# Kernel optimization log

Hardware: AMD Instinct MI355X
Metric: run time of the kernel (lower is better)

Reference implementation:

```python
import jax, jax.numpy as jnp
import numpy as np

T, B, L, CTX, H = 512, 512, 16, 64, 128
STATE_DIM, SHOT, PID, DATA = 32, 12, 35, 23


def setup_inputs() -> dict:
    key = jax.random.key(0)
    ks = jax.random.split(key, 64)
    k = iter(ks)
    def rn(shape, s=0.1):
        return (jax.random.normal(next(k), shape) * s).astype(jnp.float32)
    xs = jax.random.normal(next(k), (T, B, DATA), jnp.float32)
    xs = xs.at[:, :, 12].set(jax.random.randint(next(k), (T, B), 0, SHOT).astype(jnp.float32))
    xs = xs.at[:, :, 17].set(jax.random.randint(next(k), (T, B), 0, PID).astype(jnp.float32))
    xs = xs.at[:, :, 20].set(jax.random.randint(next(k), (T, B), 0, SHOT).astype(jnp.float32))
    return dict(
        total_xs=jnp.zeros((1,), jnp.float32),
        xs=xs,
        ts=jnp.linspace(0.0, 2.0, T).astype(jnp.float32),
        noise_std=jnp.asarray(0.1, jnp.float32),
        z0_noise=jax.random.normal(next(k), (B, L), jnp.float32),
        bm_noise=jax.random.normal(next(k), (T - 1, B, L), jnp.float32),
        shot_emb=rn((SHOT, 8)), player_emb=rn((PID, 8)),
        gru_wih=rn((3 * H, STATE_DIM)), gru_whh=rn((3 * H, H)),
        gru_bih=rn((3 * H,)), gru_bhh=rn((3 * H,)),
        enc_w=rn((CTX, H)), enc_b=rn((CTX,)),
        qz0_w=rn((2 * L, CTX)), qz0_b=rn((2 * L,)),
        f_w1=rn((H, L + CTX)), f_b1=rn((H,)), f_w2=rn((H, H)), f_b2=rn((H,)),
        f_w3=rn((L, H)), f_b3=rn((L,)),
        h_w1=rn((H, L)), h_b1=rn((H,)), h_w2=rn((H, H)), h_b2=rn((H,)),
        h_w3=rn((L, H)), h_b3=rn((L,)),
        g_w1=rn((L, H)), g_b1=rn((L, H)), g_w2=rn((L, H)), g_b2=rn((L,)),
        proj_w=rn((STATE_DIM, L)), proj_b=rn((STATE_DIM,)),
        pz0_mean=jnp.zeros((1, L), jnp.float32), pz0_logstd=jnp.zeros((1, L), jnp.float32),
        act_w=rn((128, L)), act_b=rn((128,)),
        act_land_w=rn((2, 128)), act_shot_w=rn((SHOT, 128)), act_move_w=rn((2, 128)),
    )


def _forward(xs, noise_std, shot_emb, player_emb, gru_wih, gru_whh, gru_bih, gru_bhh,
             enc_w, enc_b, qz0_w, qz0_b,
             f_w1, f_b1, f_w2, f_b2, f_w3, f_b3,
             h_w1, h_b1, h_w2, h_b2, h_w3, h_b3,
             g_w1, g_b1, g_w2, g_b2,
             proj_w, proj_b, pz0_mean, pz0_logstd,
             act_w, act_b, act_land_w, act_shot_w, act_move_w,
             ts, z0_noise, bm_noise):
    # --- SDE_embed_and_transform: replace shot/player id cols with embeddings ---
    state = xs[:, :, :18]
    shot_ids = state[:, :, 12].astype(jnp.int32)
    pid_ids = state[:, :, 17].astype(jnp.int32)
    state_t = jnp.concatenate([state[:, :, :12], shot_emb[shot_ids],
                               state[:, :, 13:17], player_emb[pid_ids]], axis=-1)  # (T,B,32)
    xs_t = jnp.concatenate([state_t, xs[:, :, 18:]], axis=-1)  # (T,B,37)
    # --- Encoder: GRU over time-reversed states, linear head, flip back ---
    def gru_step(h, xt):
        gi = xt @ gru_wih.T + gru_bih
        gh = h @ gru_whh.T + gru_bhh
        ir, iz, inn = jnp.split(gi, 3, axis=-1)
        hr, hz, hn = jnp.split(gh, 3, axis=-1)
        r = jax.nn.sigmoid(ir + hr)
        zg = jax.nn.sigmoid(iz + hz)
        n = jnp.tanh(inn + r * hn)
        hnew = (1.0 - zg) * n + zg * h
        return hnew, hnew
    h0 = jnp.zeros((xs.shape[1], gru_whh.shape[1]), xs.dtype)
    _, hs = jax.lax.scan(gru_step, h0, state_t[::-1])
    ctx = (hs @ enc_w.T + enc_b)[::-1]  # (T,B,CTX)
    # --- posterior z0 ---
    qm, qls = jnp.split(ctx[0] @ qz0_w.T + qz0_b, 2, axis=1)
    z0 = qm + jnp.exp(qls) * z0_noise
    # --- Euler-Maruyama with logqp; searchsorted(right) -> ctx[min(i+1,T-1)] = ctx[i+1] ---
    dts = ts[1:] - ts[:-1]  # (T-1,)
    dW = jnp.sqrt(dts)[:, None, None] * bm_noise
    ctx_steps = ctx[1:]
    def mlp3(x, w1, b1, w2, b2, w3, b3):
        h1 = jax.nn.softplus(x @ w1.T + b1)
        h2 = jax.nn.softplus(h1 @ w2.T + b2)
        return h2 @ w3.T + b3
    def g_diag(y):  # (B,L): per-latent-dim scalar nets, batched over L
        hg = jax.nn.softplus(y[:, :, None] * g_w1[None] + g_b1[None])  # (B,L,H)
        return jax.nn.sigmoid(jnp.einsum('blh,lh->bl', hg, g_w2) + g_b2)
    def sde_step(z, inp):
        c, dw, dt = inp
        f_val = mlp3(jnp.concatenate([z, c], axis=1), f_w1, f_b1, f_w2, f_b2, f_w3, f_b3)
        h_val = mlp3(z, h_w1, h_b1, h_w2, h_b2, h_w3, h_b3)
        g_val = g_diag(z)
        u = (f_val - h_val) / g_val
        logr = 0.5 * jnp.sum(u * u, axis=1) * dt
        z_new = z + f_val * dt + g_val * dw
        return z_new, (z_new, logr)
    _, (z_tail, log_ratio) = jax.lax.scan(sde_step, z0, (ctx_steps, dW, dts))
    zs = jnp.concatenate([z0[None], z_tail], axis=0)  # (T,B,L)
    _xs = zs @ proj_w.T + proj_b  # (T,B,32)
    # --- action model losses ---
    a = jax.nn.relu(zs @ act_w.T + act_b)
    land = (a @ act_land_w.T).reshape(-1, 2)
    shot_logits = (a @ act_shot_w.T).reshape(-1, act_shot_w.shape[0])
    move = (a @ act_move_w.T).reshape(-1, 2)
    true_actions = xs_t[:, :, -5:]
    true_land = true_actions[:, :, :2].reshape(-1, 2)
    true_move = true_actions[:, :, 3:].reshape(-1, 2)
    true_shot = true_actions[:, :, 2].astype(jnp.int32).reshape(-1)
    land_loss = jnp.mean((land - true_land) ** 2)
    move_loss = jnp.mean((move - true_move) ** 2)
    logp = jax.nn.log_softmax(shot_logits, axis=-1)
    picked = jnp.take_along_axis(logp, true_shot[:, None], axis=1)[:, 0]
    mask = (true_shot != 0).astype(logp.dtype)  # CrossEntropy ignore_index=0
    shot_loss = -jnp.sum(picked * mask) / jnp.maximum(jnp.sum(mask), 1.0)
    # --- reconstruction log-likelihood ---
    xs_state = xs_t[:, :, :STATE_DIM]
    LOG2PI = 1.8378770664093453
    log_pxs = jnp.mean(jnp.sum(
        -0.5 * ((xs_state - _xs) / noise_std) ** 2 - jnp.log(noise_std) - 0.5 * LOG2PI,
        axis=(0, 2)))
    # --- KL(q(z0) || p(z0)) ---
    var_q = jnp.exp(2.0 * qls)
    var_p = jnp.exp(2.0 * pz0_logstd)
    kl = pz0_logstd - qls + (var_q + (qm - pz0_mean) ** 2) / (2.0 * var_p) - 0.5
    logqp0 = jnp.mean(jnp.sum(kl, axis=1))
    logqp_path = jnp.mean(jnp.sum(log_ratio, axis=0))
    return log_pxs, logqp0 + logqp_path + land_loss + shot_loss + move_loss


def reference(total_xs, xs, ts, noise_std, z0_noise, bm_noise, shot_emb, player_emb,
              gru_wih, gru_whh, gru_bih, gru_bhh, enc_w, enc_b, qz0_w, qz0_b,
              f_w1, f_b1, f_w2, f_b2, f_w3, f_b3, h_w1, h_b1, h_w2, h_b2, h_w3, h_b3,
              g_w1, g_b1, g_w2, g_b2, proj_w, proj_b, pz0_mean, pz0_logstd,
              act_w, act_b, act_land_w, act_shot_w, act_move_w):
    return _forward(xs, noise_std, shot_emb, player_emb, gru_wih, gru_whh, gru_bih, gru_bhh,
                    enc_w, enc_b, qz0_w, qz0_b,
                    f_w1, f_b1, f_w2, f_b2, f_w3, f_b3,
                    h_w1, h_b1, h_w2, h_b2, h_w3, h_b3,
                    g_w1, g_b1, g_w2, g_b2,
                    proj_w, proj_b, pz0_mean, pz0_logstd,
                    act_w, act_b, act_land_w, act_shot_w, act_move_w,
                    ts, z0_noise, bm_noise)
```

## Files before the change

### kernel.cpp

```cpp
#include <hip/hip_runtime.h>
#include <cstdint>

typedef _Float16 f16;
typedef _Float16 f16x2 __attribute__((ext_vector_type(2)));

#define T_STEPS 512
#define B_SZ 512
#define LOG2PI 1.8378770664093453f

__device__ __forceinline__ void barrier_lds() {
  asm volatile("s_waitcnt lgkmcnt(0)" ::: "memory");
  __builtin_amdgcn_s_barrier();
  asm volatile("" ::: "memory");
}

__device__ __forceinline__ uint32_t packh2(float a, float b) {
  f16x2 v; v[0] = (f16)a; v[1] = (f16)b;
  return __builtin_bit_cast(uint32_t, v);
}

__device__ __forceinline__ float fdot2(uint32_t a, uint32_t b, float c) {
#if defined(__AMDGCN__) && __has_builtin(__builtin_amdgcn_fdot2)
  return __builtin_amdgcn_fdot2(__builtin_bit_cast(f16x2, a),
                                __builtin_bit_cast(f16x2, b), c, false);
#else
  f16x2 x = __builtin_bit_cast(f16x2, a), y = __builtin_bit_cast(f16x2, b);
  return c + (float)x[0] * (float)y[0] + (float)x[1] * (float)y[1];
#endif
}

#define DOT4(acc, w0, w1, w2, w3, v)                                     \
  do {                                                                   \
    acc = fdot2((w0), (v).x, acc); acc = fdot2((w1), (v).y, acc);        \
    acc = fdot2((w2), (v).z, acc); acc = fdot2((w3), (v).w, acc);        \
  } while (0)

__device__ __forceinline__ float sigmoidf_(float x) {
  return 1.0f / (1.0f + __expf(-x));
}
__device__ __forceinline__ float tanhf_(float x) {
  float ax = fabsf(x);
  float t = __expf(-2.0f * ax);
  float r = (1.0f - t) / (1.0f + t);
  return copysignf(r, x);
}
__device__ __forceinline__ float softplusf_(float x) {
  return fmaxf(x, 0.0f) + __logf(1.0f + __expf(-fabsf(x)));
}

__global__ __launch_bounds__(256) void k_embed(
    const float* __restrict__ xs, const float* __restrict__ shot_emb,
    const float* __restrict__ player_emb, f16* __restrict__ state_t,
    float* __restrict__ accums) {
  if (blockIdx.x == 0 && threadIdx.x < 16) accums[threadIdx.x] = 0.0f;
  size_t idx = (size_t)blockIdx.x * 256 + threadIdx.x;
  const float* xp = xs + idx * 23;
  f16* op = state_t + idx * 32;
  int sid = (int)xp[12];
  int pid = (int)xp[17];
#pragma unroll
  for (int i = 0; i < 12; ++i) op[i] = (f16)xp[i];
  const float* se = shot_emb + sid * 8;
#pragma unroll
  for (int i = 0; i < 8; ++i) op[12 + i] = (f16)se[i];
#pragma unroll
  for (int i = 0; i < 4; ++i) op[20 + i] = (f16)xp[13 + i];
  const float* pe = player_emb + pid * 8;
#pragma unroll
  for (int i = 0; i < 8; ++i) op[24 + i] = (f16)pe[i];
}

__global__ __launch_bounds__(256) void k_gtab(
    const float* __restrict__ gw1, const float* __restrict__ gb1,
    const float* __restrict__ gw2, const float* __restrict__ gb2,
    float* __restrict__ g_tab) {
  int gid = blockIdx.x * 256 + threadIdx.x;
  int l = gid >> 16, yi = gid & 0xffff;
  f16 hy = __builtin_bit_cast(f16, (unsigned short)yi);
  float y = (float)hy;
  const float* w1 = gw1 + l * 128;
  const float* b1 = gb1 + l * 128;
  const float* w2 = gw2 + l * 128;
  float a0 = 0.f, a1 = 0.f;
#pragma unroll 8
  for (int h = 0; h < 128; h += 2) {
    a0 = fmaf(softplusf_(fmaf(y, w1[h], b1[h])), w2[h], a0);
    a1 = fmaf(softplusf_(fmaf(y, w1[h + 1], b1[h + 1])), w2[h + 1], a1);
  }
  g_tab[gid] = sigmoidf_(a0 + a1 + gb2[l]);
}

__global__ __launch_bounds__(512) void k_gru(
    const f16* __restrict__ state_t, const float* __restrict__ wih,
    const float* __restrict__ whh, const float* __restrict__ bih,
    const float* __restrict__ bhh, const float* __restrict__ enc_w,
    const float* __restrict__ enc_b, const float* __restrict__ qz0_w,
    const float* __restrict__ qz0_b, const float* __restrict__ z0_noise,
    const float* __restrict__ pz0_mean, const float* __restrict__ pz0_logstd,
    f16* __restrict__ ctx, float* __restrict__ z0_out,
    float* __restrict__ accums) {
  __shared__ uint32_t s_x[2][16];
  __shared__ uint32_t s_h[2][64];
  __shared__ float s_gates[2 * 128 * 4];
  __shared__ float s_encp[2 * 64 * 2];
  __shared__ float s_ctx0[2][64];
  __shared__ float s_q[2][32];

  const int tid = threadIdx.x;
  const int bbase = blockIdx.x * 2;
  const uint32_t* stu = (const uint32_t*)state_t;

  uint32_t wA[64];
  uint32_t wB[16];
  float bias0 = 0.f, bias1 = 0.f, encbr = 0.f;

  if (tid < 256) {
    int g = tid >> 7, du = tid & 127;
    const float* whr = whh + (size_t)(g * 128 + du) * 128;
#pragma unroll
    for (int i = 0; i < 64; ++i) wA[i] = packh2(whr[2 * i], whr[2 * i + 1]);
    const float* wxr = wih + (size_t)(g * 128 + du) * 32;
#pragma unroll
    for (int i = 0; i < 16; ++i) wB[i] = packh2(wxr[2 * i], wxr[2 * i + 1]);
    bias0 = bih[g * 128 + du] + bhh[g * 128 + du];
  } else if (tid < 384) {
    int du = tid - 256;
    const float* whr = whh + (size_t)(256 + du) * 128;
#pragma unroll
    for (int i = 0; i < 64; ++i) wA[i] = packh2(whr[2 * i], whr[2 * i + 1]);
    const float* wxr = wih + (size_t)(256 + du) * 32;
#pragma unroll
    for (int i = 0; i < 16; ++i) wB[i] = packh2(wxr[2 * i], wxr[2 * i + 1]);
    bias0 = bih[256 + du];
    bias1 = bhh[256 + du];
  } else {
    int e = tid - 384, c = e & 63, ks = e >> 6;
    const float* wer = enc_w + (size_t)c * 128 + ks * 64;
#pragma unroll
    for (int i = 0; i < 32; ++i) wA[i] = packh2(wer[2 * i], wer[2 * i + 1]);
    encbr = enc_b[c];
  }

  if (tid < 128) s_h[tid >> 6][tid & 63] = 0u;
  if (tid < 32) {
    int b = tid >> 4, i = tid & 15;
    s_x[b][i] = stu[((size_t)(T_STEPS - 1) * B_SZ + bbase + b) * 16 + i];
  }
  float h_old = 0.0f;
  __syncthreads();

  for (int t = T_STEPS - 1; t >= 0; --t) {
    uint4 xpref = make_uint4(0, 0, 0, 0);
    if (tid < 256) {
      int g = tid >> 7, du = tid & 127;
#pragma unroll
      for (int b = 0; b < 2; ++b) {
        float a = bias0;
        const uint4* xq = (const uint4*)&s_x[b][0];
#pragma unroll
        for (int j = 0; j < 4; ++j) {
          uint4 v = xq[j];
          DOT4(a, wB[4 * j], wB[4 * j + 1], wB[4 * j + 2], wB[4 * j + 3], v);
        }
        const uint4* hq = (const uint4*)&s_h[b][0];
#pragma unroll
        for (int j = 0; j < 16; ++j) {
          uint4 v = hq[j];
          DOT4(a, wA[4 * j], wA[4 * j + 1], wA[4 * j + 2], wA[4 * j + 3], v);
        }
        s_gates[(b * 128 + du) * 4 + g] = a;
      }
    } else if (tid < 384) {
      int du = tid - 256;
#pragma unroll
      for (int b = 0; b < 2; ++b) {
        float aI = bias0, aH = bias1;
        const uint4* xq = (const uint4*)&s_x[b][0];
#pragma unroll
        for (int j = 0; j < 4; ++j) {
          uint4 v = xq[j];
          DOT4(aI, wB[4 * j], wB[4 * j + 1], wB[4 * j + 2], wB[4 * j + 3], v);
        }
        const uint4* hq = (const uint4*)&s_h[b][0];
#pragma unroll
        for (int j = 0; j < 16; ++j) {
          uint4 v = hq[j];
          DOT4(aH, wA[4 * j], wA[4 * j + 1], wA[4 * j + 2], wA[4 * j + 3], v);
        }
        s_gates[(b * 128 + du) * 4 + 2] = aI;
        s_gates[(b * 128 + du) * 4 + 3] = aH;
      }
    } else {
      int e = tid - 384, ks = e >> 6, cc = e & 63;
      (void)cc;
      if (t < T_STEPS - 1) {
#pragma unroll
        for (int b = 0; b < 2; ++b) {
          float a = 0.f;
          const uint4* hq = (const uint4*)&s_h[b][ks * 32];
#pragma unroll
          for (int j = 0; j < 8; ++j) {
            uint4 v = hq[j];
            DOT4(a, wA[4 * j], wA[4 * j + 1], wA[4 * j + 2], wA[4 * j + 3], v);
          }
          s_encp[(b * 64 + cc) * 2 + ks] = a;
        }
      }
      if (e < 8 && t > 0) {
        int b = e & 1, q = e >> 1;
        xpref = *(const uint4*)(stu +
                                ((size_t)(t - 1) * B_SZ + bbase + b) * 16 + q * 4);
      }
    }
    barrier_lds();
    if (tid < 256) {
      int b = tid >> 7, du = tid & 127;
      const float4 gt = *(const float4*)&s_gates[(b * 128 + du) * 4];
      float r = sigmoidf_(gt.x), zg = sigmoidf_(gt.y);
      float n = tanhf_(gt.z + r * gt.w);
      float hnew = (1.0f - zg) * n + zg * h_old;
      h_old = hnew;
      ((f16*)&s_h[b][0])[du] = (f16)hnew;
    } else if (tid >= 384) {
      int e = tid - 384, cc = e & 63, b = e >> 6;
      if (t < T_STEPS - 1) {
        float2 p = *(const float2*)&s_encp[(b * 64 + cc) * 2];
        ctx[((size_t)(t + 1) * B_SZ + bbase + b) * 64 + cc] =
            (f16)(p.x + p.y + encbr);
      }
      if (e < 8 && t > 0) {
        int b2 = e & 1, q = e >> 1;
        *(uint4*)&s_x[b2][q * 4] = xpref;
      }
    }
    barrier_lds();
  }

  if (tid >= 384) {
    int e = tid - 384, ks = e >> 6, cc = e & 63;
#pragma unroll
    for (int b = 0; b < 2; ++b) {
      float a = 0.f;
      const uint4* hq = (const uint4*)&s_h[b][ks * 32];
#pragma unroll
      for (int j = 0; j < 8; ++j) {
        uint4 v = hq[j];
        DOT4(a, wA[4 * j], wA[4 * j + 1], wA[4 * j + 2], wA[4 * j + 3], v);
      }
      s_encp[(b * 64 + cc) * 2 + ks] = a;
    }
  }
  __syncthreads();
  if (tid >= 384) {
    int e = tid - 384, cc = e & 63, b = e >> 6;
    float2 p = *(const float2*)&s_encp[(b * 64 + cc) * 2];
    float val = p.x + p.y + encbr;
    ctx[((size_t)bbase + b) * 64 + cc] = (f16)val;
    s_ctx0[b][cc] = val;
  }
  __syncthreads();
  if (tid < 64) {
    int b = tid >> 5, o = tid & 31;
    float acc = qz0_b[o];
#pragma unroll 8
    for (int k = 0; k < 64; ++k) acc += qz0_w[o * 64 + k] * s_ctx0[b][k];
    s_q[b][o] = acc;
  }
  __syncthreads();
  if (tid < 32) {
    int b = tid >> 4, l = tid & 15;
    int bg = bbase + b;
    float qm = s_q[b][l], qls = s_q[b][16 + l];
    float z0v = qm + __expf(qls) * z0_noise[bg * 16 + l];
    z0_out[bg * 16 + l] = z0v;
    float pm = pz0_mean[l], pls = pz0_logstd[l];
    float var_q = __expf(2.0f * qls);
    float var_p = __expf(2.0f * pls);
    float dm = qm - pm;
    float kl = pls - qls + (var_q + dm * dm) / (2.0f * var_p) - 0.5f;
    atomicAdd(&accums[5], kl);
  }
}

__global__ __launch_bounds__(256, 2) void k_sde(
    const f16* __restrict__ ctx, const float* __restrict__ z0_in,
    const float* __restrict__ ts, const float* __restrict__ bm_noise,
    const float* __restrict__ fw1, const float* __restrict__ fb1,
    const float* __restrict__ fw2, const float* __restrict__ fb2,
    const float* __restrict__ fw3, const float* __restrict__ fb3,
    const float* __restrict__ hw1, const float* __restrict__ hb1,
    const float* __restrict__ hw2, const float* __restrict__ hb2,
    const float* __restrict__ hw3, const float* __restrict__ hb3,
    const float* __restrict__ g_tab,
    f16* __restrict__ zs, float* __restrict__ accums) {
  __shared__ uint32_t s_x2[40];
  __shared__ uint32_t s_h1[2][64];
  __shared__ uint32_t s_h2[2][64];
  __shared__ float s_dts[T_STEPS];

  const int tid = threadIdx.x;
  const int bg = blockIdx.x;
  const uint32_t* cu = (const uint32_t*)ctx;
  const int l = tid >> 2;
  const bool zlane = (tid < 64) && ((tid & 3) == 0);

  uint32_t uw1[40];
  uint32_t wP2[64];
  uint32_t wP3[32];
  float bias1r = 0.f, bias2r = 0.f, fb3r = 0.f, hb3r = 0.f;

  if (tid < 128) {
    const float* w = fw1 + (size_t)tid * 80;
#pragma unroll
    for (int i = 0; i < 40; ++i) uw1[i] = packh2(w[2 * i], w[2 * i + 1]);
    bias1r = fb1[tid];
  } else {
    int u = tid - 128;
    const float* w = hw1 + (size_t)u * 16;
#pragma unroll
    for (int i = 0; i < 8; ++i) uw1[i] = packh2(w[2 * i], w[2 * i + 1]);
    bias1r = hb1[u];
  }
  {
    int mlp = tid >> 7, u = tid & 127;
    const float* w = (mlp ? hw2 : fw2) + (size_t)u * 128;
#pragma unroll
    for (int i = 0; i < 64; ++i) wP2[i] = packh2(w[2 * i], w[2 * i + 1]);
    bias2r = (mlp ? hb2 : fb2)[u];
  }
  if (tid < 64) {
    int mlp = (tid >> 1) & 1, kh = tid & 1;
    const float* w = (mlp ? hw3 : fw3) + (size_t)l * 128 + kh * 64;
#pragma unroll
    for (int i = 0; i < 32; ++i) wP3[i] = packh2(w[2 * i], w[2 * i + 1]);
    if ((tid & 3) == 0) {
      fb3r = fb3[l];
      hb3r = hb3[l];
    }
  }

  for (int i = tid; i < T_STEPS - 1; i += 256) s_dts[i] = ts[i + 1] - ts[i];
  float zreg = 0.f, bmc = 0.f, path_acc = 0.f;
  uint4 cpref = make_uint4(0, 0, 0, 0);
  if (zlane) {
    zreg = z0_in[bg * 16 + l];
    ((f16*)&s_x2[0])[l] = (f16)zreg;
    zs[(size_t)bg * 16 + l] = (f16)zreg;
    bmc = bm_noise[(size_t)bg * 16 + l];
  }
  if (tid >= 128 && tid < 136) {
    int q = tid - 128;
    uint4 v = *(const uint4*)(cu + ((size_t)1 * B_SZ + bg) * 32 + q * 4);
    *(uint4*)&s_x2[8 + q * 4] = v;
  }
  __syncthreads();

  for (int t = 0; t < T_STEPS - 1; ++t) {
    float bmn = 0.f, gvp = 0.f;
    if (zlane) {
      unsigned short zb = __builtin_bit_cast(unsigned short, (f16)zreg);
      gvp = g_tab[l * 65536 + (int)zb];
      if (t < T_STEPS - 2)
        bmn = bm_noise[((size_t)(t + 1) * B_SZ + bg) * 16 + l];
    }
    if (tid >= 128 && tid < 136 && t <= T_STEPS - 3) {
      int q = tid - 128;
      cpref = *(const uint4*)(cu + ((size_t)(t + 2) * B_SZ + bg) * 32 + q * 4);
    }
    if (tid < 128) {
      float a0 = bias1r, a1 = 0.f;
      const uint4* xq = (const uint4*)&s_x2[0];
#pragma unroll
      for (int j = 0; j < 10; j += 2) {
        uint4 v0 = xq[j], v1 = xq[j + 1];
        DOT4(a0, uw1[4 * j], uw1[4 * j + 1], uw1[4 * j + 2], uw1[4 * j + 3], v0);
        DOT4(a1, uw1[4 * j + 4], uw1[4 * j + 5], uw1[4 * j + 6], uw1[4 * j + 7], v1);
      }
      ((f16*)&s_h1[0][0])[tid] = (f16)softplusf_(a0 + a1);
    } else {
      float a = bias1r;
      const uint4* xq = (const uint4*)&s_x2[0];
#pragma unroll
      for (int j = 0; j < 2; ++j) {
        uint4 v = xq[j];
        DOT4(a, uw1[4 * j], uw1[4 * j + 1], uw1[4 * j + 2], uw1[4 * j + 3], v);
      }
      ((f16*)&s_h1[1][0])[tid - 128] = (f16)softplusf_(a);
    }
    barrier_lds();
    {
      int mlp = tid >> 7, u = tid & 127;
      float a0 = 0.f, a1 = 0.f;
      const uint4* hq = (const uint4*)&s_h1[mlp][0];
#pragma unroll
      for (int j = 0; j < 16; j += 2) {
        uint4 v0 = hq[j], v1 = hq[j + 1];
        DOT4(a0, wP2[4 * j], wP2[4 * j + 1], wP2[4 * j + 2], wP2[4 * j + 3], v0);
        DOT4(a1, wP2[4 * j + 4], wP2[4 * j + 5], wP2[4 * j + 6], wP2[4 * j + 7], v1);
      }
      ((f16*)&s_h2[mlp][0])[u] = (f16)softplusf_(a0 + a1 + bias2r);
    }
    barrier_lds();
    if (tid < 64) {
      int kh = tid & 1;
      int mlp = (tid >> 1) & 1;
      const uint4* hq = (const uint4*)&s_h2[mlp][kh * 32];
      float a0 = 0.f, a1 = 0.f;
#pragma unroll
      for (int j = 0; j < 8; j += 2) {
        uint4 v0 = hq[j], v1 = hq[j + 1];
        DOT4(a0, wP3[4 * j], wP3[4 * j + 1], wP3[4 * j + 2], wP3[4 * j + 3], v0);
        DOT4(a1, wP3[4 * j + 4], wP3[4 * j + 5], wP3[4 * j + 6], wP3[4 * j + 7], v1);
      }
      float a = a0 + a1;
      float full = a + __shfl_xor(a, 1);
      float other = __shfl_xor(full, 2);
      if ((tid & 3) == 0) {
        float fv = full + fb3r;
        float hv = other + hb3r;
        float gv = gvp;
        float dt = s_dts[t];
        float u_ = (fv - hv) / gv;
        float lsum = u_ * u_;
        lsum += __shfl_xor(lsum, 4);
        lsum += __shfl_xor(lsum, 8);
        lsum += __shfl_xor(lsum, 16);
        lsum += __shfl_xor(lsum, 32);
        if (tid == 0) path_acc += 0.5f * lsum * dt;
        float dw = sqrtf(dt) * bmc;
        float zn = zreg + fv * dt + gv * dw;
        zreg = zn;
        ((f16*)&s_x2[0])[l] = (f16)zn;
        zs[((size_t)(t + 1) * B_SZ + bg) * 16 + l] = (f16)zn;
        bmc = bmn;
      }
    } else if (tid >= 128 && tid < 136 && t <= T_STEPS - 3) {
      int q = tid - 128;
      *(uint4*)&s_x2[8 + q * 4] = cpref;
    }
    barrier_lds();
  }
  if (tid == 0) atomicAdd(&accums[6], path_acc);
}

__global__ __launch_bounds__(256) void k_dec(
    const f16* __restrict__ zs, const f16* __restrict__ state_t,
    const float* __restrict__ xs, const float* __restrict__ proj_w,
    const float* __restrict__ proj_b, const float* __restrict__ act_w,
    const float* __restrict__ act_b, const float* __restrict__ land_w,
    const float* __restrict__ shot_w, const float* __restrict__ move_w,
    float* __restrict__ accums) {
  __shared__ uint32_t s_proj[8 * 32];
  __shared__ uint32_t s_act[8 * 128];
  __shared__ uint32_t s_head[128 * 8];
  __shared__ float s_pb[32], s_ab[128];
  __shared__ float s_red[4 * 5];

  const int tid = threadIdx.x;
  for (int id = tid; id < 8 * 32; id += 256) {
    int kp = id & 7, n = id >> 3;
    s_proj[kp * 32 + n] = packh2(proj_w[n * 16 + 2 * kp], proj_w[n * 16 + 2 * kp + 1]);
  }
  for (int id = tid; id < 8 * 128; id += 256) {
    int kp = id & 7, n = id >> 3;
    s_act[kp * 128 + n] = packh2(act_w[n * 16 + 2 * kp], act_w[n * 16 + 2 * kp + 1]);
  }
  for (int id = tid; id < 128 * 8; id += 256) {
    int j = id >> 3, p = id & 7;
    int h0 = 2 * p, h1 = 2 * p + 1;
    float w0 = (h0 < 2) ? land_w[h0 * 128 + j]
                        : (h0 < 14 ? shot_w[(h0 - 2) * 128 + j]
                                   : move_w[(h0 - 14) * 128 + j]);
    float w1 = (h1 < 2) ? land_w[h1 * 128 + j]
                        : (h1 < 14 ? shot_w[(h1 - 2) * 128 + j]
                                   : move_w[(h1 - 14) * 128 + j]);
    s_head[j * 8 + p] = packh2(w0, w1);
  }
  if (tid < 32) s_pb[tid] = proj_b[tid];
  if (tid < 128) s_ab[tid] = act_b[tid];
  __syncthreads();

  size_t idx = (size_t)blockIdx.x * 256 + tid;
  uint32_t z2[8];
  const uint32_t* zp = (const uint32_t*)(zs + idx * 16);
#pragma unroll
  for (int i = 0; i < 8; ++i) z2[i] = zp[i];
  uint32_t stv[16];
  const uint32_t* stp = (const uint32_t*)(state_t + idx * 32);
#pragma unroll
  for (int i = 0; i < 16; ++i) stv[i] = stp[i];

  float sqsum = 0.0f;
#pragma unroll 4
  for (int i = 0; i < 32; ++i) {
    float acc = s_pb[i];
#pragma unroll
    for (int kp = 0; kp < 8; ++kp) acc = fdot2(s_proj[kp * 32 + i], z2[kp], acc);
    f16x2 sv = __builtin_bit_cast(f16x2, stv[i >> 1]);
    float d = (float)sv[i & 1] - acc;
    sqsum += d * d;
  }

  float hd[16];
#pragma unroll
  for (int i = 0; i < 16; ++i) hd[i] = 0.0f;
#pragma unroll 2
  for (int j = 0; j < 128; ++j) {
    float a = s_ab[j];
#pragma unroll
    for (int kp = 0; kp < 8; ++kp) a = fdot2(s_act[kp * 128 + j], z2[kp], a);
    a = fmaxf(a, 0.0f);
#pragma unroll
    for (int p = 0; p < 8; ++p) {
      f16x2 w = __builtin_bit_cast(f16x2, s_head[j * 8 + p]);
      hd[2 * p] += (float)w[0] * a;
      hd[2 * p + 1] += (float)w[1] * a;
    }
  }
  const float* xp = xs + idx * 23;
  float dl0 = hd[0] - xp[18], dl1 = hd[1] - xp[19];
  float land = dl0 * dl0 + dl1 * dl1;
  float dm0 = hd[14] - xp[21], dm1 = hd[15] - xp[22];
  float move = dm0 * dm0 + dm1 * dm1;
  int sid = (int)xp[20];
  float m = hd[2];
#pragma unroll
  for (int s = 1; s < 12; ++s) m = fmaxf(m, hd[2 + s]);
  float sume = 0.0f;
#pragma unroll
  for (int s = 0; s < 12; ++s) sume += __expf(hd[2 + s] - m);
  float lse = m + __logf(sume);
  float pl = 0.0f;
#pragma unroll
  for (int s = 0; s < 12; ++s)
    if (s == sid) pl = hd[2 + s];
  float picked = 0.0f, cnt = 0.0f;
  if (sid != 0) {
    picked = pl - lse;
    cnt = 1.0f;
  }
  float vals[5] = {sqsum, land, move, picked, cnt};
#pragma unroll
  for (int v = 0; v < 5; ++v) {
    float x = vals[v];
    for (int off = 1; off < 64; off <<= 1) x += __shfl_xor(x, off);
    vals[v] = x;
  }
  int lane = tid & 63, wv = tid >> 6;
  if (lane == 0) {
#pragma unroll
    for (int v = 0; v < 5; ++v) s_red[wv * 5 + v] = vals[v];
  }
  __syncthreads();
  if (tid == 0) {
#pragma unroll
    for (int v = 0; v < 5; ++v) {
      float s = s_red[v] + s_red[5 + v] + s_red[10 + v] + s_red[15 + v];
      atomicAdd(&accums[v], s);
    }
  }
}

__global__ void k_fin(const float* __restrict__ accums,
                      const float* __restrict__ noise_std,
                      float* __restrict__ out) {
  if (threadIdx.x == 0 && blockIdx.x == 0) {
    float sd = noise_std[0];
    float log_pxs = -0.5f * accums[0] / (sd * sd * (float)B_SZ) -
                    (float)T_STEPS * 32.0f * (logf(sd) + 0.5f * LOG2PI);
    float land = accums[1] / (float)(T_STEPS * B_SZ * 2);
    float move = accums[2] / (float)(T_STEPS * B_SZ * 2);
    float shot = -accums[3] / fmaxf(accums[4], 1.0f);
    float out1 = accums[5] / (float)B_SZ + accums[6] / (float)B_SZ + land + shot + move;
    out[0] = log_pxs;
    out[1] = out1;
  }
}

extern "C" void kernel_launch(void* const* d_in, const int* in_sizes, int n_in,
                              void* d_out, int out_size, void* d_ws,
                              size_t ws_size, hipStream_t stream) {
  const float* xs = (const float*)d_in[1];
  const float* ts = (const float*)d_in[2];
  const float* noise_std = (const float*)d_in[3];
  const float* z0_noise = (const float*)d_in[4];
  const float* bm_noise = (const float*)d_in[5];
  const float* shot_emb = (const float*)d_in[6];
  const float* player_emb = (const float*)d_in[7];
  const float* gru_wih = (const float*)d_in[8];
  const float* gru_whh = (const float*)d_in[9];
  const float* gru_bih = (const float*)d_in[10];
  const float* gru_bhh = (const float*)d_in[11];
  const float* enc_w = (const float*)d_in[12];
  const float* enc_b = (const float*)d_in[13];
  const float* qz0_w = (const float*)d_in[14];
  const float* qz0_b = (const float*)d_in[15];
  const float* f_w1 = (const float*)d_in[16];
  const float* f_b1 = (const float*)d_in[17];
  const float* f_w2 = (const float*)d_in[18];
  const float* f_b2 = (const float*)d_in[19];
  const float* f_w3 = (const float*)d_in[20];
  const float* f_b3 = (const float*)d_in[21];
  const float* h_w1 = (const float*)d_in[22];
  const float* h_b1 = (const float*)d_in[23];
  const float* h_w2 = (const float*)d_in[24];
  const float* h_b2 = (const float*)d_in[25];
  const float* h_w3 = (const float*)d_in[26];
  const float* h_b3 = (const float*)d_in[27];
  const float* g_w1 = (const float*)d_in[28];
  const float* g_b1 = (const float*)d_in[29];
  const float* g_w2 = (const float*)d_in[30];
  const float* g_b2 = (const float*)d_in[31];
  const float* proj_w = (const float*)d_in[32];
  const float* proj_b = (const float*)d_in[33];
  const float* pz0_mean = (const float*)d_in[34];
  const float* pz0_logstd = (const float*)d_in[35];
  const float* act_w = (const float*)d_in[36];
  const float* act_b = (const float*)d_in[37];
  const float* act_land_w = (const float*)d_in[38];
  const float* act_shot_w = (const float*)d_in[39];
  const float* act_move_w = (const float*)d_in[40];

  char* ws = (char*)d_ws;
  float* accums = (float*)ws;
  f16* state_t = (f16*)(ws + 256);
  f16* ctx = (f16*)(ws + 256 + 16777216);
  float* z0b = (float*)(ws + 256 + 16777216 + 33554432);
  f16* zs = (f16*)(ws + 256 + 16777216 + 33554432 + 32768);
  float* g_tab = (float*)(ws + 256 + 16777216 + 33554432 + 32768 + 8388608);

  k_embed<<<1024, 256, 0, stream>>>(xs, shot_emb, player_emb, state_t, accums);
  k_gtab<<<4096, 256, 0, stream>>>(g_w1, g_b1, g_w2, g_b2, g_tab);
  k_gru<<<256, 512, 0, stream>>>(state_t, gru_wih, gru_whh, gru_bih, gru_bhh,
                                 enc_w, enc_b, qz0_w, qz0_b, z0_noise, pz0_mean,
                                 pz0_logstd, ctx, z0b, accums);
  k_sde<<<512, 256, 0, stream>>>(ctx, z0b, ts, bm_noise, f_w1, f_b1, f_w2, f_b2,
                                 f_w3, f_b3, h_w1, h_b1, h_w2, h_b2, h_w3, h_b3,
                                 g_tab, zs, accums);
  k_dec<<<1024, 256, 0, stream>>>(zs, state_t, xs, proj_w, proj_b, act_w, act_b,
                                  act_land_w, act_shot_w, act_move_w, accums);
  k_fin<<<1, 64, 0, stream>>>(accums, noise_std, (float*)d_out);
}
```

Baseline: 1.686 ms.

## Cut per-step barriers in GRU and SDE loops via double buffering and redundant gate compute

The GRU loop now double-buffers its gate and input tiles and has every thread recompute the gate nonlinearity for the hidden units it needs, which removes one barrier per timestep. The SDE loop follows the same idea: the third-layer drift, the z update and the ctx staging are folded into the next step's first phase, so each step has two barriers instead of three. The first-layer MLP work is split across all 256 threads in pairs combined with shuffles, and the third-layer weights move into LDS. The cost is redundant transcendental work and extra LDS traffic, and the sequential dependency chain is reordered, so correctness depends on the buffer indexing being right.

```diff
diff --git a/kernel.cpp b/kernel.cpp
--- a/kernel.cpp
+++ b/kernel.cpp
@@ -99,14 +99,14 @@
     const float* __restrict__ pz0_mean, const float* __restrict__ pz0_logstd,
     f16* __restrict__ ctx, float* __restrict__ z0_out,
     float* __restrict__ accums) {
-  __shared__ uint32_t s_x[2][16];
+  __shared__ uint32_t s_x[2][2][16];
   __shared__ uint32_t s_h[2][64];
-  __shared__ float s_gates[2 * 128 * 4];
-  __shared__ float s_encp[2 * 64 * 2];
+  __shared__ float s_g[2][4][2][128];
   __shared__ float s_ctx0[2][64];
   __shared__ float s_q[2][32];
 
   const int tid = threadIdx.x;
+  const int ln = tid & 63;
   const int bbase = blockIdx.x * 2;
   const uint32_t* stu = (const uint32_t*)state_t;
 
@@ -134,48 +134,74 @@
     bias0 = bih[256 + du];
     bias1 = bhh[256 + du];
   } else {
-    int e = tid - 384, c = e & 63, ks = e >> 6;
+    int e = tid - 384, c = e >> 1, ks = e & 1;
     const float* wer = enc_w + (size_t)c * 128 + ks * 64;
 #pragma unroll
     for (int i = 0; i < 32; ++i) wA[i] = packh2(wer[2 * i], wer[2 * i + 1]);
     encbr = enc_b[c];
   }
 
+  float ho[2][2] = {{0.f, 0.f}, {0.f, 0.f}};
   if (tid < 128) s_h[tid >> 6][tid & 63] = 0u;
   if (tid < 32) {
     int b = tid >> 4, i = tid & 15;
-    s_x[b][i] = stu[((size_t)(T_STEPS - 1) * B_SZ + bbase + b) * 16 + i];
-  }
-  float h_old = 0.0f;
+    s_x[1][b][i] = stu[((size_t)(T_STEPS - 1) * B_SZ + bbase + b) * 16 + i];
+  }
   __syncthreads();
 
   for (int t = T_STEPS - 1; t >= 0; --t) {
+    const int p = t & 1;
     uint4 xpref = make_uint4(0, 0, 0, 0);
+    if (tid >= 368 && tid < 376 && t > 0) {
+      int i = tid - 368, b = i & 1, q = i >> 1;
+      xpref = *(const uint4*)(stu +
+                              ((size_t)(t - 1) * B_SZ + bbase + b) * 16 + q * 4);
+    }
+    if (t != T_STEPS - 1) {
+#pragma unroll
+      for (int b = 0; b < 2; ++b) {
+        float2 G0 = *(const float2*)&s_g[p ^ 1][0][b][2 * ln];
+        float2 G1 = *(const float2*)&s_g[p ^ 1][1][b][2 * ln];
+        float2 G2 = *(const float2*)&s_g[p ^ 1][2][b][2 * ln];
+        float2 G3 = *(const float2*)&s_g[p ^ 1][3][b][2 * ln];
+        float r0 = sigmoidf_(G0.x), zg0 = sigmoidf_(G1.x);
+        float n0 = tanhf_(G2.x + r0 * G3.x);
+        float h0 = (1.0f - zg0) * n0 + zg0 * ho[b][0];
+        ho[b][0] = h0;
+        float r1 = sigmoidf_(G0.y), zg1 = sigmoidf_(G1.y);
+        float n1 = tanhf_(G2.y + r1 * G3.y);
+        float h1 = (1.0f - zg1) * n1 + zg1 * ho[b][1];
+        ho[b][1] = h1;
+        s_h[b][ln] = packh2(h0, h1);
+      }
+    }
     if (tid < 256) {
       int g = tid >> 7, du = tid & 127;
 #pragma unroll
       for (int b = 0; b < 2; ++b) {
-        float a = bias0;
-        const uint4* xq = (const uint4*)&s_x[b][0];
-#pragma unroll
-        for (int j = 0; j < 4; ++j) {
-          uint4 v = xq[j];
-          DOT4(a, wB[4 * j], wB[4 * j + 1], wB[4 * j + 2], wB[4 * j + 3], v);
+        float a0 = bias0, a1 = 0.f;
+        const uint4* xq = (const uint4*)&s_x[p][b][0];
+#pragma unroll
+        for (int j = 0; j < 4; j += 2) {
+          uint4 v0 = xq[j], v1 = xq[j + 1];
+          DOT4(a0, wB[4 * j], wB[4 * j + 1], wB[4 * j + 2], wB[4 * j + 3], v0);
+          DOT4(a1, wB[4 * j + 4], wB[4 * j + 5], wB[4 * j + 6], wB[4 * j + 7], v1);
         }
         const uint4* hq = (const uint4*)&s_h[b][0];
 #pragma unroll
-        for (int j = 0; j < 16; ++j) {
-          uint4 v = hq[j];
-          DOT4(a, wA[4 * j], wA[4 * j + 1], wA[4 * j + 2], wA[4 * j + 3], v);
+        for (int j = 0; j < 16; j += 2) {
+          uint4 v0 = hq[j], v1 = hq[j + 1];
+          DOT4(a0, wA[4 * j], wA[4 * j + 1], wA[4 * j + 2], wA[4 * j + 3], v0);
+          DOT4(a1, wA[4 * j + 4], wA[4 * j + 5], wA[4 * j + 6], wA[4 * j + 7], v1);
         }
-        s_gates[(b * 128 + du) * 4 + g] = a;
+        s_g[p][g][b][du] = a0 + a1;
       }
     } else if (tid < 384) {
       int du = tid - 256;
 #pragma unroll
       for (int b = 0; b < 2; ++b) {
-        float aI = bias0, aH = bias1;
-        const uint4* xq = (const uint4*)&s_x[b][0];
+        float aI = bias0, aH0 = bias1, aH1 = 0.f;
+        const uint4* xq = (const uint4*)&s_x[p][b][0];
 #pragma unroll
         for (int j = 0; j < 4; ++j) {
           uint4 v = xq[j];
@@ -183,80 +209,80 @@
         }
         const uint4* hq = (const uint4*)&s_h[b][0];
 #pragma unroll
-        for (int j = 0; j < 16; ++j) {
-          uint4 v = hq[j];
-          DOT4(aH, wA[4 * j], wA[4 * j + 1], wA[4 * j + 2], wA[4 * j + 3], v);
+        for (int j = 0; j < 16; j += 2) {
+          uint4 v0 = hq[j], v1 = hq[j + 1];
+          DOT4(aH0, wA[4 * j], wA[4 * j + 1], wA[4 * j + 2], wA[4 * j + 3], v0);
+          DOT4(aH1, wA[4 * j + 4], wA[4 * j + 5], wA[4 * j + 6], wA[4 * j + 7], v1);
         }
-        s_gates[(b * 128 + du) * 4 + 2] = aI;
-        s_gates[(b * 128 + du) * 4 + 3] = aH;
+        s_g[p][2][b][du] = aI;
+        s_g[p][3][b][du] = aH0 + aH1;
       }
     } else {
-      int e = tid - 384, ks = e >> 6, cc = e & 63;
-      (void)cc;
+      int e = tid - 384, c = e >> 1, ks = e & 1;
+      (void)c;
       if (t < T_STEPS - 1) {
 #pragma unroll
         for (int b = 0; b < 2; ++b) {
-          float a = 0.f;
+          float a0 = 0.f, a1 = 0.f;
           const uint4* hq = (const uint4*)&s_h[b][ks * 32];
 #pragma unroll
-          for (int j = 0; j < 8; ++j) {
-            uint4 v = hq[j];
-            DOT4(a, wA[4 * j], wA[4 * j + 1], wA[4 * j + 2], wA[4 * j + 3], v);
+          for (int j = 0; j < 8; j += 2) {
+            uint4 v0 = hq[j], v1 = hq[j + 1];
+            DOT4(a0, wA[4 * j], wA[4 * j + 1], wA[4 * j + 2], wA[4 * j + 3], v0);
+            DOT4(a1, wA[4 * j + 4], wA[4 * j + 5], wA[4 * j + 6], wA[4 * j + 7], v1);
           }
-          s_encp[(b * 64 + cc) * 2 + ks] = a;
+          float a = a0 + a1;
+          float full = a + __shfl_xor(a, 1);
+          if (ks == 0)
+            ctx[((size_t)(t + 1) * B_SZ + bbase + b) * 64 + c] =
+                (f16)(full + encbr);
         }
       }
-      if (e < 8 && t > 0) {
-        int b = e & 1, q = e >> 1;
-        xpref = *(const uint4*)(stu +
-                                ((size_t)(t - 1) * B_SZ + bbase + b) * 16 + q * 4);
-      }
+    }
+    if (tid >= 368 && tid < 376 && t > 0) {
+      int i = tid - 368, b = i & 1, q = i >> 1;
+      *(uint4*)&s_x[p ^ 1][b][q * 4] = xpref;
     }
     barrier_lds();
-    if (tid < 256) {
-      int b = tid >> 7, du = tid & 127;
-      const float4 gt = *(const float4*)&s_gates[(b * 128 + du) * 4];
-      float r = sigmoidf_(gt.x), zg = sigmoidf_(gt.y);
-      float n = tanhf_(gt.z + r * gt.w);
-      float hnew = (1.0f - zg) * n + zg * h_old;
-      h_old = hnew;
-      ((f16*)&s_h[b][0])[du] = (f16)hnew;
-    } else if (tid >= 384) {
-      int e = tid - 384, cc = e & 63, b = e >> 6;
-      if (t < T_STEPS - 1) {
-        float2 p = *(const float2*)&s_encp[(b * 64 + cc) * 2];
-        ctx[((size_t)(t + 1) * B_SZ + bbase + b) * 64 + cc] =
-            (f16)(p.x + p.y + encbr);
-      }
-      if (e < 8 && t > 0) {
-        int b2 = e & 1, q = e >> 1;
-        *(uint4*)&s_x[b2][q * 4] = xpref;
-      }
-    }
-    barrier_lds();
-  }
-
-  if (tid >= 384) {
-    int e = tid - 384, ks = e >> 6, cc = e & 63;
+  }
+
+  {
 #pragma unroll
     for (int b = 0; b < 2; ++b) {
-      float a = 0.f;
-      const uint4* hq = (const uint4*)&s_h[b][ks * 32];
-#pragma unroll
-      for (int j = 0; j < 8; ++j) {
-        uint4 v = hq[j];
-        DOT4(a, wA[4 * j], wA[4 * j + 1], wA[4 * j + 2], wA[4 * j + 3], v);
-      }
-      s_encp[(b * 64 + cc) * 2 + ks] = a;
+      float2 G0 = *(const float2*)&s_g[0][0][b][2 * ln];
+      float2 G1 = *(const float2*)&s_g[0][1][b][2 * ln];
+      float2 G2 = *(const float2*)&s_g[0][2][b][2 * ln];
+      float2 G3 = *(const float2*)&s_g[0][3][b][2 * ln];
+      float r0 = sigmoidf_(G0.x), zg0 = sigmoidf_(G1.x);
+      float n0 = tanhf_(G2.x + r0 * G3.x);
+      float h0 = (1.0f - zg0) * n0 + zg0 * ho[b][0];
+      float r1 = sigmoidf_(G0.y), zg1 = sigmoidf_(G1.y);
+      float n1 = tanhf_(G2.y + r1 * G3.y);
+      float h1 = (1.0f - zg1) * n1 + zg1 * ho[b][1];
+      s_h[b][ln] = packh2(h0, h1);
     }
   }
   __syncthreads();
   if (tid >= 384) {
-    int e = tid - 384, cc = e & 63, b = e >> 6;
-    float2 p = *(const float2*)&s_encp[(b * 64 + cc) * 2];
-    float val = p.x + p.y + encbr;
-    ctx[((size_t)bbase + b) * 64 + cc] = (f16)val;
-    s_ctx0[b][cc] = val;
+    int e = tid - 384, c = e >> 1, ks = e & 1;
+#pragma unroll
+    for (int b = 0; b < 2; ++b) {
+      float a0 = 0.f, a1 = 0.f;
+      const uint4* hq = (const uint4*)&s_h[b][ks * 32];
+#pragma unroll
+      for (int j = 0; j < 8; j += 2) {
+        uint4 v0 = hq[j], v1 = hq[j + 1];
+        DOT4(a0, wA[4 * j], wA[4 * j + 1], wA[4 * j + 2], wA[4 * j + 3], v0);
+        DOT4(a1, wA[4 * j + 4], wA[4 * j + 5], wA[4 * j + 6], wA[4 * j + 7], v1);
+      }
+      float a = a0 + a1;
+      float full = a + __shfl_xor(a, 1);
+      if (ks == 0) {
+        float val = full + encbr;
+        ctx[((size_t)bbase + b) * 64 + c] = (f16)val;
+        s_ctx0[b][c] = val;
+      }
+    }
   }
   __syncthreads();
   if (tid < 64) {
@@ -293,152 +319,192 @@
     const float* __restrict__ hw3, const float* __restrict__ hb3,
     const float* __restrict__ g_tab,
     f16* __restrict__ zs, float* __restrict__ accums) {
-  __shared__ uint32_t s_x2[40];
+  __shared__ uint32_t s_x2[2][40];
   __shared__ uint32_t s_h1[2][64];
   __shared__ uint32_t s_h2[2][64];
+  __shared__ uint4 s_w3[8][64];
   __shared__ float s_dts[T_STEPS];
 
   const int tid = threadIdx.x;
+  const int lane = tid & 63;
   const int bg = blockIdx.x;
-  const uint32_t* cu = (const uint32_t*)ctx;
-  const int l = tid >> 2;
-  const bool zlane = (tid < 64) && ((tid & 3) == 0);
-
-  uint32_t uw1[40];
-  uint32_t wP2[64];
-  uint32_t wP3[32];
-  float bias1r = 0.f, bias2r = 0.f, fb3r = 0.f, hb3r = 0.f;
-
-  if (tid < 128) {
-    const float* w = fw1 + (size_t)tid * 80;
-#pragma unroll
-    for (int i = 0; i < 40; ++i) uw1[i] = packh2(w[2 * i], w[2 * i + 1]);
-    bias1r = fb1[tid];
-  } else {
-    int u = tid - 128;
-    const float* w = hw1 + (size_t)u * 16;
-#pragma unroll
-    for (int i = 0; i < 8; ++i) uw1[i] = packh2(w[2 * i], w[2 * i + 1]);
-    bias1r = hb1[u];
-  }
+  const uint4* ctx4 = (const uint4*)ctx;
+
+  const int r1 = tid >> 1, hh = tid & 1;
+  const int mlp = tid >> 7, u2 = tid & 127;
+  const int r3 = lane >> 1;
+  const int net3 = r3 >> 4;
+  const int l3 = r3 & 15;
+  const int hh3 = lane & 1;
+  const bool zlane = (net3 == 0) && (hh3 == 0);
+  const bool stg = (tid >= 32 && tid < 40);
+
+  uint32_t uw1f[20], uw1h[4], wP2[64];
+  float bf1r, bh1r, bias2r, fb3r, hb3r;
   {
-    int mlp = tid >> 7, u = tid & 127;
-    const float* w = (mlp ? hw2 : fw2) + (size_t)u * 128;
+    const float* w = fw1 + (size_t)r1 * 80 + hh * 40;
+#pragma unroll
+    for (int i = 0; i < 20; ++i) uw1f[i] = packh2(w[2 * i], w[2 * i + 1]);
+    bf1r = fb1[r1];
+  }
+  {
+    const float* w = hw1 + (size_t)r1 * 16 + hh * 8;
+#pragma unroll
+    for (int i = 0; i < 4; ++i) uw1h[i] = packh2(w[2 * i], w[2 * i + 1]);
+    bh1r = hb1[r1];
+  }
+  {
+    const float* w = (mlp ? hw2 : fw2) + (size_t)u2 * 128;
 #pragma unroll
     for (int i = 0; i < 64; ++i) wP2[i] = packh2(w[2 * i], w[2 * i + 1]);
-    bias2r = (mlp ? hb2 : fb2)[u];
-  }
+    bias2r = (mlp ? hb2 : fb2)[u2];
+  }
+  fb3r = fb3[l3];
+  hb3r = hb3[l3];
   if (tid < 64) {
-    int mlp = (tid >> 1) & 1, kh = tid & 1;
-    const float* w = (mlp ? hw3 : fw3) + (size_t)l * 128 + kh * 64;
-#pragma unroll
-    for (int i = 0; i < 32; ++i) wP3[i] = packh2(w[2 * i], w[2 * i + 1]);
-    if ((tid & 3) == 0) {
-      fb3r = fb3[l];
-      hb3r = hb3[l];
-    }
-  }
-
+    const float* w = (net3 ? hw3 : fw3) + (size_t)l3 * 128 + hh3 * 64;
+#pragma unroll
+    for (int j = 0; j < 8; ++j) {
+      uint4 q;
+      q.x = packh2(w[8 * j + 0], w[8 * j + 1]);
+      q.y = packh2(w[8 * j + 2], w[8 * j + 3]);
+      q.z = packh2(w[8 * j + 4], w[8 * j + 5]);
+      q.w = packh2(w[8 * j + 6], w[8 * j + 7]);
+      s_w3[j][tid] = q;
+    }
+  }
   for (int i = tid; i < T_STEPS - 1; i += 256) s_dts[i] = ts[i + 1] - ts[i];
-  float zreg = 0.f, bmc = 0.f, path_acc = 0.f;
+
+  float zreg = 0.f, bmc = 0.f, bmn = 0.f, gvp = 0.f, path_acc = 0.f;
   uint4 cpref = make_uint4(0, 0, 0, 0);
   if (zlane) {
-    zreg = z0_in[bg * 16 + l];
-    ((f16*)&s_x2[0])[l] = (f16)zreg;
-    zs[(size_t)bg * 16 + l] = (f16)zreg;
-    bmc = bm_noise[(size_t)bg * 16 + l];
-  }
-  if (tid >= 128 && tid < 136) {
-    int q = tid - 128;
-    uint4 v = *(const uint4*)(cu + ((size_t)1 * B_SZ + bg) * 32 + q * 4);
-    *(uint4*)&s_x2[8 + q * 4] = v;
+    zreg = z0_in[bg * 16 + l3];
+    ((f16*)&s_x2[0][0])[l3] = (f16)zreg;
+    if (tid < 64) zs[(size_t)bg * 16 + l3] = (f16)zreg;
+    bmc = bm_noise[(size_t)bg * 16 + l3];
+    bmn = bm_noise[((size_t)1 * B_SZ + bg) * 16 + l3];
+    unsigned short zb = __builtin_bit_cast(unsigned short, (f16)zreg);
+    gvp = g_tab[l3 * 65536 + (int)zb];
+  }
+  if (stg) {
+    int q = tid - 32;
+    uint4 v = ctx4[((size_t)1 * B_SZ + bg) * 8 + q];
+    *(uint4*)&s_x2[0][8 + q * 4] = v;
   }
   __syncthreads();
 
   for (int t = 0; t < T_STEPS - 1; ++t) {
-    float bmn = 0.f, gvp = 0.f;
-    if (zlane) {
-      unsigned short zb = __builtin_bit_cast(unsigned short, (f16)zreg);
-      gvp = g_tab[l * 65536 + (int)zb];
-      if (t < T_STEPS - 2)
-        bmn = bm_noise[((size_t)(t + 1) * B_SZ + bg) * 16 + l];
-    }
-    if (tid >= 128 && tid < 136 && t <= T_STEPS - 3) {
-      int q = tid - 128;
-      cpref = *(const uint4*)(cu + ((size_t)(t + 2) * B_SZ + bg) * 32 + q * 4);
-    }
-    if (tid < 128) {
-      float a0 = bias1r, a1 = 0.f;
-      const uint4* xq = (const uint4*)&s_x2[0];
-#pragma unroll
-      for (int j = 0; j < 10; j += 2) {
-        uint4 v0 = xq[j], v1 = xq[j + 1];
-        DOT4(a0, uw1[4 * j], uw1[4 * j + 1], uw1[4 * j + 2], uw1[4 * j + 3], v0);
-        DOT4(a1, uw1[4 * j + 4], uw1[4 * j + 5], uw1[4 * j + 6], uw1[4 * j + 7], v1);
-      }
-      ((f16*)&s_h1[0][0])[tid] = (f16)softplusf_(a0 + a1);
-    } else {
-      float a = bias1r;
-      const uint4* xq = (const uint4*)&s_x2[0];
-#pragma unroll
-      for (int j = 0; j < 2; ++j) {
-        uint4 v = xq[j];
-        DOT4(a, uw1[4 * j], uw1[4 * j + 1], uw1[4 * j + 2], uw1[4 * j + 3], v);
-      }
-      ((f16*)&s_h1[1][0])[tid - 128] = (f16)softplusf_(a);
+    const int p = t & 1;
+    if (stg && t <= T_STEPS - 3)
+      cpref = ctx4[((size_t)(t + 2) * B_SZ + bg) * 8 + (tid - 32)];
+    if (t > 0) {
+      const uint4* hq = (const uint4*)&s_h2[net3][hh3 * 32];
+      float a0 = 0.f, a1 = 0.f;
+#pragma unroll
+      for (int j = 0; j < 8; j += 2) {
+        uint4 w0 = s_w3[j][lane], w1v = s_w3[j + 1][lane];
+        uint4 v0 = hq[j], v1 = hq[j + 1];
+        DOT4(a0, w0.x, w0.y, w0.z, w0.w, v0);
+        DOT4(a1, w1v.x, w1v.y, w1v.z, w1v.w, v1);
+      }
+      float a = a0 + a1;
+      float full = a + __shfl_xor(a, 1);
+      float cross = __shfl_xor(full, 32);
+      if (zlane) {
+        float fv = full + fb3r;
+        float hv = cross + hb3r;
+        float gv = gvp;
+        float dt = s_dts[t - 1];
+        float u_ = (fv - hv) / gv;
+        float ls = u_ * u_;
+        ls += __shfl_xor(ls, 2);
+        ls += __shfl_xor(ls, 4);
+        ls += __shfl_xor(ls, 8);
+        ls += __shfl_xor(ls, 16);
+        if (tid == 0) path_acc += 0.5f * ls * dt;
+        float dw = sqrtf(dt) * bmc;
+        float zn = zreg + fv * dt + gv * dw;
+        zreg = zn;
+        ((f16*)&s_x2[p][0])[l3] = (f16)zn;
+        if (tid < 64) zs[((size_t)t * B_SZ + bg) * 16 + l3] = (f16)zn;
+        bmc = bmn;
+        if (t <= T_STEPS - 3)
+          bmn = bm_noise[((size_t)(t + 1) * B_SZ + bg) * 16 + l3];
+        unsigned short zb = __builtin_bit_cast(unsigned short, (f16)zn);
+        gvp = g_tab[l3 * 65536 + (int)zb];
+      }
+    }
+    {
+      const uint4* xq = (const uint4*)&s_x2[p][0];
+      const int base = hh * 5;
+      float a0 = 0.f, a1 = 0.f;
+      {
+        uint4 v0 = xq[base + 0], v1 = xq[base + 1];
+        DOT4(a0, uw1f[0], uw1f[1], uw1f[2], uw1f[3], v0);
+        DOT4(a1, uw1f[4], uw1f[5], uw1f[6], uw1f[7], v1);
+        uint4 v2 = xq[base + 2], v3 = xq[base + 3];
+        DOT4(a0, uw1f[8], uw1f[9], uw1f[10], uw1f[11], v2);
+        DOT4(a1, uw1f[12], uw1f[13], uw1f[14], uw1f[15], v3);
+        uint4 v4 = xq[base + 4];
+        DOT4(a0, uw1f[16], uw1f[17], uw1f[18], uw1f[19], v4);
+      }
+      float af = a0 + a1;
+      uint4 vz = xq[hh];
+      float ah = 0.f;
+      DOT4(ah, uw1h[0], uw1h[1], uw1h[2], uw1h[3], vz);
+      float ff = af + __shfl_xor(af, 1);
+      float fh = ah + __shfl_xor(ah, 1);
+      if (hh == 0)
+        ((f16*)&s_h1[0][0])[r1] = (f16)softplusf_(ff + bf1r);
+      else
+        ((f16*)&s_h1[1][0])[r1] = (f16)softplusf_(fh + bh1r);
     }
     barrier_lds();
     {
-      int mlp = tid >> 7, u = tid & 127;
+      const uint4* hq = (const uint4*)&s_h1[mlp][0];
       float a0 = 0.f, a1 = 0.f;
-      const uint4* hq = (const uint4*)&s_h1[mlp][0];
 #pragma unroll
       for (int j = 0; j < 16; j += 2) {
         uint4 v0 = hq[j], v1 = hq[j + 1];
         DOT4(a0, wP2[4 * j], wP2[4 * j + 1], wP2[4 * j + 2], wP2[4 * j + 3], v0);
         DOT4(a1, wP2[4 * j + 4], wP2[4 * j + 5], wP2[4 * j + 6], wP2[4 * j + 7], v1);
       }
-      ((f16*)&s_h2[mlp][0])[u] = (f16)softplusf_(a0 + a1 + bias2r);
-    }
+      ((f16*)&s_h2[mlp][0])[u2] = (f16)softplusf_(a0 + a1 + bias2r);
+    }
+    if (stg && t <= T_STEPS - 3)
+      *(uint4*)&s_x2[p ^ 1][8 + (tid - 32) * 4] = cpref;
     barrier_lds();
-    if (tid < 64) {
-      int kh = tid & 1;
-      int mlp = (tid >> 1) & 1;
-      const uint4* hq = (const uint4*)&s_h2[mlp][kh * 32];
-      float a0 = 0.f, a1 = 0.f;
-#pragma unroll
-      for (int j = 0; j < 8; j += 2) {
-        uint4 v0 = hq[j], v1 = hq[j + 1];
-        DOT4(a0, wP3[4 * j], wP3[4 * j + 1], wP3[4 * j + 2], wP3[4 * j + 3], v0);
-        DOT4(a1, wP3[4 * j + 4], wP3[4 * j + 5], wP3[4 * j + 6], wP3[4 * j + 7], v1);
-      }
-      float a = a0 + a1;
-      float full = a + __shfl_xor(a, 1);
-      float other = __shfl_xor(full, 2);
-      if ((tid & 3) == 0) {
-        float fv = full + fb3r;
-        float hv = other + hb3r;
-        float gv = gvp;
-        float dt = s_dts[t];
-        float u_ = (fv - hv) / gv;
-        float lsum = u_ * u_;
-        lsum += __shfl_xor(lsum, 4);
-        lsum += __shfl_xor(lsum, 8);
-        lsum += __shfl_xor(lsum, 16);
-        lsum += __shfl_xor(lsum, 32);
-        if (tid == 0) path_acc += 0.5f * lsum * dt;
-        float dw = sqrtf(dt) * bmc;
-        float zn = zreg + fv * dt + gv * dw;
-        zreg = zn;
-        ((f16*)&s_x2[0])[l] = (f16)zn;
-        zs[((size_t)(t + 1) * B_SZ + bg) * 16 + l] = (f16)zn;
-        bmc = bmn;
-      }
-    } else if (tid >= 128 && tid < 136 && t <= T_STEPS - 3) {
-      int q = tid - 128;
-      *(uint4*)&s_x2[8 + q * 4] = cpref;
-    }
-    barrier_lds();
+  }
+
+  if (tid < 64) {
+    const uint4* hq = (const uint4*)&s_h2[net3][hh3 * 32];
+    float a0 = 0.f, a1 = 0.f;
+#pragma unroll
+    for (int j = 0; j < 8; j += 2) {
+      uint4 w0 = s_w3[j][lane], w1v = s_w3[j + 1][lane];
+      uint4 v0 = hq[j], v1 = hq[j + 1];
+      DOT4(a0, w0.x, w0.y, w0.z, w0.w, v0);
+      DOT4(a1, w1v.x, w1v.y, w1v.z, w1v.w, v1);
+    }
+    float a = a0 + a1;
+    float full = a + __shfl_xor(a, 1);
+    float cross = __shfl_xor(full, 32);
+    if (zlane) {
+      float fv = full + fb3r;
+      float hv = cross + hb3r;
+      float gv = gvp;
+      float dt = s_dts[T_STEPS - 2];
+      float u_ = (fv - hv) / gv;
+      float ls = u_ * u_;
+      ls += __shfl_xor(ls, 2);
+      ls += __shfl_xor(ls, 4);
+      ls += __shfl_xor(ls, 8);
+      ls += __shfl_xor(ls, 16);
+      if (tid == 0) path_acc += 0.5f * ls * dt;
+      float dw = sqrtf(dt) * bmc;
+      float zn = zreg + fv * dt + gv * dw;
+      zs[((size_t)(T_STEPS - 1) * B_SZ + bg) * 16 + l3] = (f16)zn;
+    }
   }
   if (tid == 0) atomicAdd(&accums[6], path_acc);
 }
```

Result: slower. 2.198 ms (+30.4%).
